# Optimization experiments

Measured on AMD Instinct MI355X. Metric: run time of the kernel, lower is better.

## Reference

```python
import jax, jax.numpy as jnp
import numpy as np

B, T, N = 4, 6, 1024          # patients, visits, diagnosis codes
CS, GS, H, AT, DA = 48, 32, 270, 32, 64  # code_size, graph_size, hidden, t_attention, dot-attn size
E, L, EV, ED = 32, 32, 20000, 400        # events/visit, event seq len, event vocab, event emb dim
OUT = 4000
INV_SQRT_AT = 1.0 / float(np.sqrt(AT))


def _w(k, shape, s=0.1):
    return jax.random.normal(k, shape, jnp.float32) * s


def setup_inputs():
    key = jax.random.key(0)
    ks = jax.random.split(key, 40)
    cat = jax.random.randint(ks[0], (B, T, N), 0, 4)  # disjoint m1/m2/m3 masks
    return {
        'code_x': jax.random.randint(ks[1], (B, T, N), 0, 2).astype(jnp.int32),
        'divided': jnp.stack([cat == 1, cat == 2, cat == 3], axis=-1).astype(jnp.int32),
        'neighbors': jax.random.randint(ks[2], (B, T, N), 0, 2).astype(jnp.int32),
        'lens': jnp.full((B,), T, dtype=jnp.int32),
        'events': jax.random.randint(ks[3], (B, T, E, L), 0, EV).astype(jnp.int32),
        'c_emb': _w(ks[4], (N, CS)),
        'n_emb': _w(ks[5], (N, CS)),
        'u_emb': _w(ks[6], (N, GS)),
        'adj': (jax.random.uniform(ks[7], (N, N)) < 0.02).astype(jnp.float32),
        'Wg': _w(ks[8], (CS, GS), 0.05), 'bg': jnp.zeros((GS,), jnp.float32),
        'gru_Wih': _w(ks[9], (GS, 3 * H), 0.05),
        'gru_Whh': _w(ks[10], (H, 3 * H), 0.05),
        'gru_bih': jnp.zeros((3 * H,), jnp.float32),
        'gru_bhh': jnp.zeros((3 * H,), jnp.float32),
        'Wq': _w(ks[11], (GS, AT), 0.05), 'bq': jnp.zeros((AT,), jnp.float32),
        'Wk': _w(ks[12], (GS, AT), 0.05), 'bk': jnp.zeros((AT,), jnp.float32),
        'Wv': _w(ks[13], (GS, H), 0.05), 'bv': jnp.zeros((H,), jnp.float32),
        'Wd': _w(ks[14], (H, DA), 0.05), 'bd': jnp.zeros((DA,), jnp.float32),
        'ctx': _w(ks[15], (DA,), 0.1),
        'Eemb': _w(ks[16], (EV, ED), 0.1),
        'lstm_Wih': _w(ks[17], (ED, 4 * H), 0.05),
        'lstm_Whh': _w(ks[18], (H, 4 * H), 0.05),
        'lstm_b': jnp.zeros((4 * H,), jnp.float32),
        'Wc': _w(ks[19], (H, OUT), 0.05),
        'bc': jnp.zeros((OUT,), jnp.float32),
    }


def _forward(code_x, divided, neighbors, events,
             c_emb, n_emb, u_emb, adj, Wg, bg,
             gru_Wih, gru_Whh, gru_bih, gru_bhh,
             Wq, bq, Wk, bk, Wv, bv,
             Wd, bd, ctx,
             Eemb, lstm_Wih, lstm_Whh, lstm_b,
             Wc, bc):
    Bsz, Tn, Nn = code_x.shape
    Hh = gru_Whh.shape[0]
    cx = code_x.astype(jnp.float32)
    nb = neighbors.astype(jnp.float32)
    dv = divided.astype(jnp.float32)

    def gru_cell(x, h):  # torch GRUCell: gates in (r, z, n) order
        gi = x @ gru_Wih + gru_bih
        gh = h @ gru_Whh + gru_bhh
        ir, iz, i_n = jnp.split(gi, 3, axis=-1)
        hr, hz, h_n = jnp.split(gh, 3, axis=-1)
        r = jax.nn.sigmoid(ir + hr)
        z = jax.nn.sigmoid(iz + hz)
        n = jnp.tanh(i_n + r * h_n)
        return (1.0 - z) * n + z * h

    def visit_step(carry, xs):
        h_prev, no_prev = carry
        t, c_t, n_t, d_t = xs  # c_t/n_t: [B,N], d_t: [B,N,3]
        cm = c_t[..., None]
        nm = n_t[..., None]
        # GraphLayer
        ce = cm * c_emb  # [B,N,CS]
        ne = nm * n_emb
        Ace = jnp.einsum('mn,bnc->bmc', adj, ce)
        Ane = jnp.einsum('mn,bnc->bmc', adj, ne)
        co = jax.nn.leaky_relu((ce + cm * Ace + cm * Ane) @ Wg + bg)  # [B,N,GS]
        no = jax.nn.leaky_relu((ne + nm * Ane + nm * Ace) @ Wg + bg)
        m1 = d_t[..., 0] > 0
        m2 = d_t[..., 1] > 0
        m3 = d_t[..., 2] > 0
        # TransitionLayer: persistent codes (m1) -> GRU, masked max-pool
        h_m1 = gru_cell(co, h_prev)  # [B,N,H]
        has1 = jnp.any(m1, axis=1, keepdims=True)
        mx1 = jnp.max(jnp.where(m1[..., None], h_m1, -jnp.inf), axis=1)
        out_m1 = jnp.where(has1, mx1, 0.0)
        # emerging (m2) / unrelated (m3) codes -> single-head attention over the m23 set
        m23 = m2 | m3
        q_in = jnp.where(m3[..., None], u_emb, no_prev)  # [B,N,GS]
        q = q_in @ Wq + bq
        k = co @ Wk + bk
        v = co @ Wv + bv
        g = jnp.einsum('bia,bja->bij', q, k) * INV_SQRT_AT  # [B,N,N]
        has23 = jnp.any(m23, axis=1)  # [B]
        g = jnp.where(m23[:, None, :], g, -jnp.inf)
        g = jnp.where(has23[:, None, None], g, 0.0)  # keep softmax finite when m23 empty
        score = jax.nn.softmax(g, axis=-1)
        h_m23 = jnp.tanh(jnp.einsum('bij,bjh->bih', score, v))  # [B,N,H]
        valid23 = (t > 0) & has23
        mx23 = jnp.max(jnp.where(m23[..., None], h_m23, -jnp.inf), axis=1)
        out_m23 = jnp.where(valid23[:, None], mx23, 0.0)
        h_new = jnp.where(m1[..., None], h_m1, 0.0)
        h_new = jnp.where(((t > 0) & m23)[..., None], h_m23, h_new)
        return (h_new, no), out_m1 + out_m23

    h0 = jnp.zeros((Bsz, Nn, Hh), jnp.float32)
    no0 = jnp.zeros((Bsz, Nn, GS), jnp.float32)
    xs = (jnp.arange(Tn), jnp.swapaxes(cx, 0, 1), jnp.swapaxes(nb, 0, 1), jnp.swapaxes(dv, 0, 1))
    _, outs = jax.lax.scan(visit_step, (h0, no0), xs)
    out_last = outs[-1]  # only the last visit's output survives the original loop

    # SentimentModel: embedding + LSTM over last visit's events (seqs == padded length L)
    x_emb = Eemb[events[:, -1]]  # [B,E,L,ED]

    def lstm_step(carry, x_t):  # torch LSTM gate order (i, f, g, o)
        h, c = carry
        gates = x_t @ lstm_Wih + h @ lstm_Whh + lstm_b
        i, f, gg, o = jnp.split(gates, 4, axis=-1)
        c = jax.nn.sigmoid(f) * c + jax.nn.sigmoid(i) * jnp.tanh(gg)
        h = jax.nn.sigmoid(o) * jnp.tanh(c)
        return (h, c), None

    hc0 = (jnp.zeros((Bsz, E, Hh), jnp.float32), jnp.zeros((Bsz, E, Hh), jnp.float32))
    (h_ev, _), _ = jax.lax.scan(lstm_step, hc0, jnp.moveaxis(x_emb, 2, 0))  # [B,E,H]

    def dp_attention(x):  # x: [B,M,H] -> [B,H]
        vu = (x @ Wd + bd) @ ctx  # [B,M]
        s = jax.nn.softmax(vu, axis=-1)
        return jnp.sum(x * s[..., None], axis=-2)

    stacked = jnp.concatenate([out_last[:, None, :], h_ev], axis=1)  # [B,1+E,H]
    o1 = dp_attention(stacked)
    o2 = dp_attention(o1[:, None, :])  # softmax over a singleton -> identity (as in source)
    return jax.nn.sigmoid(o2 @ Wc + bc)  # [B,OUT]


def reference(code_x, divided, neighbors, lens, events,
              c_emb, n_emb, u_emb, adj, Wg, bg,
              gru_Wih, gru_Whh, gru_bih, gru_bhh,
              Wq, bq, Wk, bk, Wv, bv,
              Wd, bd, ctx,
              Eemb, lstm_Wih, lstm_Whh, lstm_b,
              Wc, bc):
    # lens is all-T (fixed number of visits per patient in this reference)
    return _forward(code_x, divided, neighbors, events,
                    c_emb, n_emb, u_emb, adj, Wg, bg,
                    gru_Wih, gru_Whh, gru_bih, gru_bhh,
                    Wq, bq, Wk, bk, Wv, bv,
                    Wd, bd, ctx,
                    Eemb, lstm_Wih, lstm_Whh, lstm_b,
                    Wc, bc)
```

## Files before the change

kernel.cpp:

```cpp
#include <hip/hip_runtime.h>
#include <hip/hip_bf16.h>
#include <math.h>

#define Bc   4
#define Tc   6
#define Nc   1024
#define CSc  48
#define GSc  32
#define Hc   270
#define ATc  32
#define DAc  64
#define Ec   32
#define Lc   32
#define EDc  400
#define OUTc 4000
#define H3c  810
#define H4c  1080
#define BEc  128
#define KPE  416
#define KPG  64
#define KAB  320
#define NCMB 1382
#define NZCAP 96
#define INV_SQRT_AT_F 0.17677669529663687f
// ... 104 lines not shown
        for (int mi=0;mi<4;mi++) af[mi]  = *(const s8v*)&As[(wm+mi*16+lr)*40 + lk];
        #pragma unroll
        for (int ni=0;ni<4;ni++) bfr[ni] = *(const s8v*)&Bs[(wn+ni*16+lr)*40 + lk];
        #pragma unroll
        for (int mi=0;mi<4;mi++)
          #pragma unroll
          for (int ni=0;ni<4;ni++)
            acc[mi][ni] = __builtin_amdgcn_mfma_f32_16x16x32_bf16(af[mi], bfr[ni], acc[mi][ni], 0,0,0);
        __syncthreads();
    }

    #pragma unroll
    for (int mi=0;mi<4;mi++){
      #pragma unroll
      for (int ni=0;ni<4;ni++){
        int col = n0+wn+ni*16+lr;
        if (col >= N) continue;
        float bv_ = bias ? bias[col] : 0.0f;
        #pragma unroll
        for (int r=0;r<4;r++){
          int row = m0+wm+mi*16+lq*4+r;
          if (row >= M) continue;
          float x = acc[mi][ni][r] + bv_;
          if (EPIL == 0){
              float* C = (float*)P0;
              size_t base = (SPLITK>0) ? (size_t)z*(size_t)sC : 0;
              size_t grow = (SPLITK>0) ? (size_t)row : (size_t)z*M + row;
              C[base + grow*ldc + col] = x;
          } else if (EPIL == 1){
              x = (x>0.0f) ? x : 0.01f*x;
              if (row < 4096) ((ushort_t*)P0)[(size_t)row*KAB + col] = f2bf(x);
              else            ((ushort_t*)P1)[(size_t)(row-4096)*32 + col] = f2bf(x);
          } else if (EPIL == 5){
              if (col < 32)        ((ushort_t*)P0)[(size_t)row*32 + col] = f2bf(x);
              else if (col < 302)  ((ushort_t*)P1)[(size_t)(col-32)*4096 + row] = f2bf(x);
              else                 ((float*)P2)[(size_t)row*H4c + (col-302)] = x;
          }
        }
      }
    }
}

__global__ __launch_bounds__(256)
void attn_fused_kernel(const ushort_t* __restrict__ no_prev, const ushort_t* __restrict__ u_embb,
                       const float* __restrict__ Wq, const float* __restrict__ bq,
                       const ushort_t* __restrict__ kb, const ushort_t* __restrict__ vT,
                       const int* __restrict__ divided, const float* __restrict__ hm1,
                       ushort_t* __restrict__ Abuf, float* __restrict__ hm23,
                       int t, int wr23)
{
    __shared__ float    scs[16*1028];
    __shared__ ushort_t stg[288*72];
    __shared__ ushort_t Qs[16*40];
    __shared__ float    qinS[16*33];
    __shared__ float    WqS[32*33];
    __shared__ float    mskS[1024];
    __shared__ float    rowmax[16], rowinv[16], hasS[4];

    const int rt = blockIdx.x;
    const int b  = blockIdx.y;
    const int tid = threadIdx.x;
    const int w = tid>>6, l = tid&63, lr = l&15, lq = l>>4;
    const int lk8 = lq*8;
    const int row0 = rt*16;
    const size_t gq = (size_t)b*Nc + row0;

    bool lany = false;
    #pragma unroll
    for (int c4=0;c4<4;c4++){
        int c = tid*4 + c4;
        const int* dv = divided + (((size_t)b*Tc + t)*Nc + c)*3;
        bool m23 = (dv[1]>0)||(dv[2]>0);
        mskS[c] = m23 ? 1.0f : 0.0f;
        lany |= m23;
    }
    if (l==0) hasS[w] = 0.0f;
    bool wany = __any(lany);
    if (l==0) hasS[w] = wany ? 1.0f : 0.0f;

    for (int i=tid;i<16*32;i+=256){
        int r = i>>5, j = i&31;
        int n = row0 + r;
        bool m3 = divided[(((size_t)b*Tc+t)*Nc+n)*3+2] > 0;
        qinS[r*33+j] = m3 ? b2f(u_embb[(size_t)n*GSc+j]) : b2f(no_prev[(gq+r)*GSc+j]);
    }
    for (int i=tid;i<32*32;i+=256){
        int j=i>>5, o=i&31;
        WqS[j*33+o] = Wq[(size_t)j*ATc+o];
    }
    __syncthreads();
    const bool has = (hasS[0]+hasS[1]+hasS[2]+hasS[3]) > 0.5f;

    {
        int r = tid>>4, o2 = (tid&15)*2;
        float a0 = bq[o2], a1 = bq[o2+1];
        for (int j=0;j<32;j++){
            float q = qinS[r*33+j];
            a0 += q*WqS[j*33+o2];
            a1 += q*WqS[j*33+o2+1];
        }
        Qs[r*40+o2]   = f2bf(a0);
        Qs[r*40+o2+1] = f2bf(a1);
    }
    __syncthreads();

    for (int kt=0;kt<8;kt++){
        #pragma unroll
        for (int i2=0;i2<2;i2++){
            int idx = tid*2+i2;
            int kr = idx>>2, seg = idx&3;
            *(uint4*)&stg[kr*40 + seg*8] =
                *(const uint4*)(kb + ((size_t)b*Nc + kt*128 + kr)*GSc + seg*8);
        }
        __syncthreads();
        s8v af = *(const s8v*)&Qs[lr*40 + lk8];
        #pragma unroll
        for (int ni=0;ni<2;ni++){
            int nt = w*2 + ni;
            s8v bf = *(const s8v*)&stg[(nt*16+lr)*40 + lk8];
            f4v a0 = (f4v){0,0,0,0};
            a0 = __builtin_amdgcn_mfma_f32_16x16x32_bf16(af, bf, a0, 0,0,0);
            #pragma unroll
            for (int r2=0;r2<4;r2++)
                scs[(lq*4+r2)*1028 + kt*128 + nt*16 + lr] = a0[r2];
        }
        __syncthreads();
    }

    {
        int r = tid>>4, i = tid&15;
        if (has){
            float m = -INFINITY;
            for (int j=0;j<64;j++){
                int c = i + 16*j;
                if (mskS[c] > 0.5f) m = fmaxf(m, scs[r*1028+c]*INV_SQRT_AT_F);
            }
            #pragma unroll
            for (int o=1;o<16;o<<=1) m = fmaxf(m, __shfl_xor(m, o, 64));
            if (i==0) rowmax[r] = m;
        }
        __syncthreads();
        float gm = has ? rowmax[r] : 0.0f;
        float s = 0.0f;
        for (int j=0;j<64;j++){
            int c = i + 16*j;
            float p;
            if (has) p = (mskS[c]>0.5f) ? expf(scs[r*1028+c]*INV_SQRT_AT_F - gm) : 0.0f;
            else     p = 1.0f;
            scs[r*1028+c] = p;
            s += p;
        }
        #pragma unroll
        for (int o=1;o<16;o<<=1) s += __shfl_xor(s, o, 64);
        if (i==0) rowinv[r] = 1.0f/s;
    }
    for (int i=tid;i<18*72;i+=256)
        stg[(270+(i/72))*72 + (i%72)] = 0;
    __syncthreads();
    const float inv = rowinv[lr];

    f4v acc[5];
    #pragma unroll
    for (int j=0;j<5;j++) acc[j] = (f4v){0,0,0,0};
    for (int vc=0;vc<16;vc++){
        for (int idx=tid; idx<2160; idx+=256){
            int n = idx>>3, seg = idx&7;
            *(uint4*)&stg[n*72 + seg*8] =
                *(const uint4*)(vT + (size_t)n*(Bc*Nc) + (size_t)b*Nc + vc*64 + seg*8);
        }
        __syncthreads();
        #pragma unroll
        for (int ki=0;ki<2;ki++){
            int kbase = vc*64 + ki*32 + lk8;
            u16x8 a16;
            #pragma unroll
            for (int e=0;e<8;e++) a16[e] = f2bf(scs[lr*1028 + kbase + e] * inv);
            s8v af = *(s8v*)&a16;
            #pragma unroll
            for (int j=0;j<5;j++){
                int nt = w + 4*j;
                if (nt < 18){
                    s8v bf = *(const s8v*)&stg[(nt*16+lr)*72 + ki*32 + lk8];
                    acc[j] = __builtin_amdgcn_mfma_f32_16x16x32_bf16(af, bf, acc[j], 0,0,0);
                }
            }
        }
        __syncthreads();
    }

    #pragma unroll
    for (int j=0;j<5;j++){
        int nt = w + 4*j;
        if (nt >= 18) continue;
        int col = nt*16 + lr;
        if (col >= Hc) continue;
        #pragma unroll
        for (int r2=0;r2<4;r2++){
            int row16 = lq*4 + r2;
            size_t grow = gq + row16;
            int n = row0 + row16;
            const int* dv = divided + (((size_t)b*Tc + t)*Nc + n)*3;
            bool m1  = dv[0]>0;
            bool m23 = (dv[1]>0)||(dv[2]>0);
            float xt = tanhf(acc[j][r2]);
            float hv = m23 ? xt : (m1 ? hm1[grow*Hc + col] : 0.0f);
            Abuf[grow*KAB + 32 + col] = f2bf(hv);
            if (wr23) hm23[grow*Hc + col] = xt;
        }
    }
}

template<int ACT>
__global__ __launch_bounds__(256)
void gemm_kernel(const float* __restrict__ A, const float* __restrict__ Bm,
                 const float* __restrict__ bias, float* __restrict__ C,
                 int M, int Nn, int K)
{
    constexpr int BM=64, BN=64, BK=16;
    __shared__ float As[BK][BM+4];
    __shared__ float Bs[BK][BN+4];
    const int row0 = blockIdx.y*BM, col0 = blockIdx.x*BN;
    const int tid = threadIdx.x;
    const int tr = (tid>>4)<<2;
    const int tc = (tid&15)<<2;
    const int ar = tid>>2;
    const int ac = (tid&3)<<2;
    const int br = tid>>4;
    const int bc = (tid&15)<<2;
    float acc[4][4] = {};
    for (int k0=0;k0<K;k0+=BK){
        #pragma unroll
        for (int i=0;i<4;i++){
            int gr=row0+ar, gc=k0+ac+i;
            As[ac+i][ar] = (gr<M && gc<K) ? A[(size_t)gr*K+gc] : 0.0f;
        }
        #pragma unroll
        for (int i=0;i<4;i++){
// ... 3 lines not shown
        __syncthreads();
        #pragma unroll
        for (int kk=0;kk<BK;kk++){
            float a0=As[kk][tr+0], a1=As[kk][tr+1], a2=As[kk][tr+2], a3=As[kk][tr+3];
            float b0=Bs[kk][tc+0], b1=Bs[kk][tc+1], b2=Bs[kk][tc+2], b3=Bs[kk][tc+3];
            acc[0][0]+=a0*b0; acc[0][1]+=a0*b1; acc[0][2]+=a0*b2; acc[0][3]+=a0*b3;
            acc[1][0]+=a1*b0; acc[1][1]+=a1*b1; acc[1][2]+=a1*b2; acc[1][3]+=a1*b3;
            acc[2][0]+=a2*b0; acc[2][1]+=a2*b1; acc[2][2]+=a2*b2; acc[2][3]+=a2*b3;
            acc[3][0]+=a3*b0; acc[3][1]+=a3*b1; acc[3][2]+=a3*b2; acc[3][3]+=a3*b3;
        }
        __syncthreads();
    }
    #pragma unroll
    for (int i=0;i<4;i++){
        int r=row0+tr+i; if (r>=M) continue;
        #pragma unroll
        for (int j=0;j<4;j++){
            int c=col0+tc+j; if (c>=Nn) continue;
            float x = acc[i][j];
            if (bias) x += bias[c];
            if (ACT==3) x = 1.0f/(1.0f+expf(-x));
            C[(size_t)r*Nn+c] = x;
        }
    }
}

#define PR0 32768LL
#define PR1 2048LL
#define PR3 442240LL
#define PR4 1382LL
#define PR5 449280LL
#define PR6 313344LL
#define PR7 73728LL
#define PR8 36864LL
#define PR9 1310720LL
#define PRTOT (PR0+PR1+PR3+PR4+PR5+PR6+PR7+PR8+PR9)

__global__ void prep_kernel(const float* __restrict__ u_emb,
                            const float* __restrict__ Wg,
                            const float* __restrict__ Wk, const float* __restrict__ Wv,
                            const float* __restrict__ gru_Wih, const float* __restrict__ gru_Whh,
                            const float* __restrict__ bk, const float* __restrict__ bv,
                            const float* __restrict__ gru_bih, const float* __restrict__ gru_bhh,
                            const float* __restrict__ lstm_Wih, const float* __restrict__ lstm_Whh,
                            ushort_t* u_embb, ushort_t* WgT,
                            ushort_t* WB, float* biasB, ushort_t* WTl, ushort_t* WhhRT,
                            ushort_t* hbLA, ushort_t* hbLB, float* cst, ushort_t* Abuf)
{
    long long idx = (long long)blockIdx.x*256 + threadIdx.x;
    if (idx < PR0){ u_embb[idx] = f2bf(u_emb[idx]); return; } idx -= PR0;
    if (idx < PR1){ int n=(int)(idx>>6), k=(int)(idx&63);
        WgT[idx] = (k<CSc) ? f2bf(Wg[(size_t)k*GSc+n]) : (ushort_t)0; return; } idx -= PR1;
    if (idx < PR3){
        int n=(int)(idx/KAB), k=(int)(idx%KAB);
        float v = 0.0f;
        if (n < 32){            if (k<32) v = Wk[(size_t)k*ATc + n]; }
        else if (n < 302){      if (k<32) v = Wv[(size_t)k*Hc + (n-32)]; }
        else if (n < 572){ int j=n-302;
            if (k<32) v = gru_Wih[(size_t)k*H3c + j];
            else if (k<302) v = gru_Whh[(size_t)(k-32)*H3c + j]; }
        else if (n < 842){ int j=(n-572)+270;
            if (k<32) v = gru_Wih[(size_t)k*H3c + j];
            else if (k<302) v = gru_Whh[(size_t)(k-32)*H3c + j]; }
        else if (n < 1112){ int j=(n-842)+540;
            if (k<32) v = gru_Wih[(size_t)k*H3c + j]; }
        else { int j=(n-1112)+540;
            if (k>=32 && k<302) v = gru_Whh[(size_t)(k-32)*H3c + j]; }
        WB[idx] = f2bf(v); return; } idx -= PR3;
    if (idx < PR4){
        int n = (int)idx; float v;
        if (n < 32)        v = bk[n];
        else if (n < 302)  v = bv[n-32];
        else if (n < 572)  v = gru_bih[n-302] + gru_bhh[n-302];
        else if (n < 842)  v = gru_bih[(n-572)+270] + gru_bhh[(n-572)+270];
        else if (n < 1112) v = gru_bih[(n-842)+540];
        else               v = gru_bhh[(n-1112)+540];
        biasB[n] = v; return; } idx -= PR4;
    if (idx < PR5){ int n=(int)(idx/KPE), k=(int)(idx%KPE);
        WTl[idx] = (k<EDc) ? f2bf(lstm_Wih[(size_t)k*H4c+n]) : (ushort_t)0; return; } idx -= PR5;
    if (idx < PR6){
        int jg=(int)(idx/(64*288)); int r2=(int)(idx%(64*288));
        int n=r2/288, k=r2%288;
        int gate=n>>4, jj=n&15, j=jg*16+jj;
        WhhRT[idx] = (k<Hc && j<Hc) ? f2bf(lstm_Whh[(size_t)k*H4c + gate*Hc + j]) : (ushort_t)0;
        return; } idx -= PR6;
    if (idx < PR7){ if (idx < 36864) hbLA[idx] = 0; else hbLB[idx-36864] = 0; return; } idx -= PR7;
    if (idx < PR8){ cst[idx] = 0.0f; return; } idx -= PR8;
    if (idx < PR9){ Abuf[idx] = 0; }
}

__global__ void nz_build_kernel(const float* __restrict__ adj, int* __restrict__ nzc,
                                int* __restrict__ nzidx)
{
    int n = blockIdx.x;
    __shared__ int cnt;
    if (threadIdx.x == 0) cnt = 0;
    __syncthreads();
    for (int k = threadIdx.x; k < Nc; k += 256){
        if (adj[(size_t)n*Nc + k] != 0.0f){
            int pos = atomicAdd(&cnt, 1);
            if (pos < NZCAP) nzidx[(size_t)n*NZCAP + pos] = k;
        }
    }
    __syncthreads();
    if (threadIdx.x == 0) nzc[n] = (cnt < NZCAP) ? cnt : NZCAP;
}

__global__ __launch_bounds__(192)
void s_sparse_kernel(const int* __restrict__ code_x, const int* __restrict__ neighbors,
                     const float* __restrict__ c_emb, const float* __restrict__ n_emb,
                     const int* __restrict__ nzc, const int* __restrict__ nzidx,
                     int t, float* __restrict__ S)
{
    int n = blockIdx.x;
    int tid = threadIdx.x;
    int b = tid / CSc, c = tid % CSc;
    int cnt = nzc[n];
    float s = 0.0f;
    for (int i=0; i<cnt; i++){
        int k = nzidx[(size_t)n*NZCAP + i];
        int cm = code_x  [((size_t)b*Tc+t)*Nc + k];
// ... 43 lines not shown
{
    int nc = blockIdx.x, b = blockIdx.y;
    int j = threadIdx.x;
    if (j >= Hc) return;
    float m1v = -INFINITY, m23v = -INFINITY;
    #pragma unroll 4
    for (int n = nc*32; n < nc*32+32; n++){
        const int* dv = divided + (((size_t)b*Tc + (Tc-1))*Nc + n)*3;
        bool m1  = dv[0] > 0;
        bool m23 = (dv[1] > 0) || (dv[2] > 0);
        size_t o = ((size_t)b*Nc+n)*Hc + j;
        if (m1)  m1v  = fmaxf(m1v,  hm1[o]);
        if (m23) m23v = fmaxf(m23v, hm23[o]);
    }
    part1 [((size_t)b*32+nc)*320 + j] = m1v;
    part23[((size_t)b*32+nc)*320 + j] = m23v;
}

__global__ __launch_bounds__(320)
void outlast_combine_kernel(const float* __restrict__ part1, const float* __restrict__ part23,
                            float* __restrict__ outlast)
{
    int b = blockIdx.x; int j = threadIdx.x;
    if (j >= Hc) return;
    float a = -INFINITY, c = -INFINITY;
    for (int nc=0;nc<32;nc++){
        a = fmaxf(a, part1 [((size_t)b*32+nc)*320 + j]);
        c = fmaxf(c, part23[((size_t)b*32+nc)*320 + j]);
    }
    outlast[(size_t)b*Hc + j] = (a==-INFINITY ? 0.0f : a) + (c==-INFINITY ? 0.0f : c);
}

__global__ __launch_bounds__(256)
void lstm_step_mfma(const float* __restrict__ gx,
                    const ushort_t* __restrict__ WhhRT,
                    const ushort_t* __restrict__ hb_in,
                    ushort_t* __restrict__ hb_out,
                    float* __restrict__ cst,
                    float* __restrict__ hev_out)
{
    int cg = blockIdx.x & 3, jg = blockIdx.x >> 2;
    int tid = threadIdx.x;
    int w = tid>>6, l = tid&63;
    int mi = w>>1, ni0 = (w&1)*2;
    int arow = cg*32 + mi*16 + (l&15);
    int koff = (l>>4)*8;
    const ushort_t* Wb = WhhRT + (size_t)jg*64*288;

    f4v acc0 = (f4v){0,0,0,0}, acc1 = (f4v){0,0,0,0};
    #pragma unroll
    for (int k0=0;k0<288;k0+=32){
        s8v a  = *(const s8v*)(hb_in + (size_t)arow*288 + k0 + koff);
        s8v b0 = *(const s8v*)(Wb + (size_t)(ni0*16 + (l&15))*288 + k0 + koff);
        s8v b1 = *(const s8v*)(Wb + (size_t)((ni0+1)*16 + (l&15))*288 + k0 + koff);
        acc0 = __builtin_amdgcn_mfma_f32_16x16x32_bf16(a, b0, acc0, 0,0,0);
        acc1 = __builtin_amdgcn_mfma_f32_16x16x32_bf16(a, b1, acc1, 0,0,0);
    }
    __shared__ float gs[32][64];
    int crow = mi*16 + (l>>4)*4;
    int ccol = l&15;
    #pragma unroll
    for (int r=0;r<4;r++){
        gs[crow+r][ni0*16 + ccol]     = acc0[r];
        gs[crow+r][(ni0+1)*16 + ccol] = acc1[r];
    }
    __syncthreads();
    #pragma unroll
    for (int p=0;p<2;p++){
        int idx = tid + p*256;
        int cl = idx>>4, jj = idx&15;
        int j = jg*16 + jj;
        if (j < Hc){
            int cell = cg*32 + cl;
            const float* g = gx + (size_t)cell*H4c;
            float ig = sigmoid_f(gs[cl][jj]      + g[j]);
            float fg = sigmoid_f(gs[cl][16+jj]   + g[Hc+j]);
            float gg = tanhf    (gs[cl][32+jj]   + g[2*Hc+j]);
            float og = sigmoid_f(gs[cl][48+jj]   + g[3*Hc+j]);
            size_t co = (size_t)cell*288 + j;
            float cn = fg*cst[co] + ig*gg;
            cst[co] = cn;
            float hn = og*tanhf(cn);
            hb_out[co] = f2bf(hn);
            if (hev_out) hev_out[(size_t)cell*Hc + j] = hn;
        }
    }
}

__global__ __launch_bounds__(256)
void heads_kernel(const float* __restrict__ outlast, const float* __restrict__ hev,
                  const float* __restrict__ Wd, const float* __restrict__ bd,
                  const float* __restrict__ ctx, float* __restrict__ o1)
{
    int b = blockIdx.x, tid = threadIdx.x;
    __shared__ float wdc[Hc+1];
    __shared__ float sc[Ec+1];
    for (int j=tid;j<Hc;j+=256){
        float s = 0.0f;
        for (int d=0;d<DAc;d++) s += Wd[(size_t)j*DAc+d]*ctx[d];
        wdc[j] = s;
    }
    if (tid == 255){
        float s = 0.0f;
        for (int d=0;d<DAc;d++) s += bd[d]*ctx[d];
        wdc[Hc] = s;
    }
    __syncthreads();
    if (tid < Ec+1){
        const float* x = (tid==0) ? (outlast + (size_t)b*Hc)
                                  : (hev + ((size_t)b*Ec + tid-1)*Hc);
        float s = wdc[Hc];
        for (int j=0;j<Hc;j++) s += x[j]*wdc[j];
        sc[tid] = s;
    }
    __syncthreads();
    if (tid == 0){
        float m = -INFINITY;
// ... 28 lines not shown
    const float* gru_Wih   = (const float*)d_in[11];
    const float* gru_Whh   = (const float*)d_in[12];
    const float* gru_bih   = (const float*)d_in[13];
    const float* gru_bhh   = (const float*)d_in[14];
    const float* Wq        = (const float*)d_in[15];
    const float* bq        = (const float*)d_in[16];
    const float* Wk        = (const float*)d_in[17];
    const float* bk        = (const float*)d_in[18];
    const float* Wv        = (const float*)d_in[19];
    const float* bv        = (const float*)d_in[20];
    const float* Wd        = (const float*)d_in[21];
    const float* bd        = (const float*)d_in[22];
    const float* ctx       = (const float*)d_in[23];
    const float* Eemb      = (const float*)d_in[24];
    const float* lstm_Wih  = (const float*)d_in[25];
    const float* lstm_Whh  = (const float*)d_in[26];
    const float* lstm_b    = (const float*)d_in[27];
    const float* Wc        = (const float*)d_in[28];
    const float* bc        = (const float*)d_in[29];
    float* out = (float*)d_out;

    float* ws = (float*)d_ws;
    size_t off = 0;
    auto alloc = [&](size_t n){ n = (n+7)&~(size_t)7; float* p = ws + off; off += n; return p; };
    auto allocU = [&](size_t n){ return (ushort_t*)alloc((n+1)/2); };

    float* hm1     = alloc((size_t)Bc*Nc*Hc);
    float* hm23    = alloc((size_t)Bc*Nc*Hc);
    float* S       = alloc((size_t)Nc*Bc*CSc);
    float* gsum    = alloc((size_t)Bc*Nc*H4c);
    ushort_t* Abuf  = allocU((size_t)Bc*Nc*KAB);
    ushort_t* noA   = allocU((size_t)Bc*Nc*GSc);
    ushort_t* noB   = allocU((size_t)Bc*Nc*GSc);
    ushort_t* kb    = allocU((size_t)Bc*Nc*ATc);
    ushort_t* vT    = allocU((size_t)Hc*Bc*Nc);
    ushort_t* u_embb= allocU((size_t)Nc*GSc);
    ushort_t* WgT   = allocU((size_t)GSc*KPG);
    ushort_t* WB    = allocU((size_t)NCMB*KAB);
    ushort_t* WTl   = allocU((size_t)H4c*KPE);
    ushort_t* WhhRT = allocU((size_t)17*64*288);
    ushort_t* hbLA  = allocU((size_t)BEc*288);
    ushort_t* hbLB  = allocU((size_t)BEc*288);
    float* cst     = alloc((size_t)BEc*288);
    float* biasB   = alloc((size_t)NCMB);
    int*   nzc     = (int*)alloc((size_t)Nc);
    int*   nzidx   = (int*)alloc((size_t)Nc*NZCAP);
    float* outlast = alloc((size_t)Bc*Hc);
    float* o1      = alloc((size_t)Bc*Hc);
    float* hev     = alloc((size_t)BEc*Hc);
    float* part1   = alloc((size_t)Bc*32*320);
    float* part23  = alloc((size_t)Bc*32*320);

    float* gatesx  = gsum;
    (void)ws_size; (void)in_sizes; (void)n_in; (void)out_size;

    {
        long long nb = (PRTOT + 255) / 256;
        prep_kernel<<<dim3((unsigned)nb), dim3(256), 0, stream>>>(
            u_emb, Wg, Wk, Wv, gru_Wih, gru_Whh, bk, bv, gru_bih, gru_bhh,
            lstm_Wih, lstm_Whh,
            u_embb, WgT, WB, biasB, WTl, WhhRT, hbLA, hbLB, cst, Abuf);
        nz_build_kernel<<<dim3(Nc), dim3(256), 0, stream>>>(adj, nzc, nzidx);
    }

    ushort_t* no_prev = noB;
    ushort_t* no_cur  = noA;
    for (int t=0; t<Tc; t++){
        s_sparse_kernel<<<dim3(Nc), dim3(192), 0, stream>>>(code_x, neighbors, c_emb, n_emb,
                                                            nzc, nzidx, t, S);
        mfma_k<1,0,2><<<dim3(1,64,1),256,0,stream>>>(
            (const ushort_t*)c_emb, WgT, bg,
            Abuf, no_cur, (void*)n_emb, S, code_x, neighbors,
            2*Bc*Nc, GSc, KPG, 0, KPG, 0, 0,0,0, t);
        mfma_k<5,0,0><<<dim3(11,32,1),256,0,stream>>>(
            Abuf, WB, biasB,
            kb, vT, gsum, nullptr, nullptr, nullptr,
            Bc*Nc, NCMB, KAB, KAB, KAB, 0, 0,0,0, 0);
        if (t == 0){
            gru_combine_t0_kernel<<<dim3(Bc*Nc), dim3(256), 0, stream>>>(gsum, divided, Abuf);
        } else {
            gru_combine_kernel<<<dim3(Bc*Nc), dim3(256), 0, stream>>>(gsum, Abuf, hm1);
            attn_fused_kernel<<<dim3(64, Bc), dim3(256), 0, stream>>>(
                no_prev, u_embb, Wq, bq, kb, vT, divided, hm1,
                Abuf, hm23, t, (t == Tc-1) ? 1 : 0);
            if (t == Tc-1){
                outlast_partial_kernel<<<dim3(32, Bc), dim3(320), 0, stream>>>(divided, hm1, hm23, part1, part23);
                outlast_combine_kernel<<<dim3(Bc), dim3(320), 0, stream>>>(part1, part23, outlast);
            }
        }
        ushort_t* tmp = no_prev; no_prev = no_cur; no_cur = tmp;
    }

    mfma_k<0,0,3><<<dim3(9,32,1),256,0,stream>>>(
        nullptr, WTl, lstm_b,
        gatesx, nullptr, nullptr, Eemb, events, nullptr,
        BEc*Lc, H4c, KPE, 0, KPE, H4c, 0,0,0, 0);
    {
        ushort_t* hin = hbLA; ushort_t* hout = hbLB;
        for (int l=0; l<Lc; l++){
            lstm_step_mfma<<<dim3(68), dim3(256), 0, stream>>>(
                gatesx + (size_t)l*BEc*H4c, WhhRT, hin, hout, cst,
                (l == Lc-1) ? hev : nullptr);
            ushort_t* tmp = hin; hin = hout; hout = tmp;
        }
    }

    heads_kernel<<<dim3(Bc), dim3(256), 0, stream>>>(outlast, hev, Wd, bd, ctx, o1);
    {
        dim3 grid((OUTc+63)/64, 1, 1);
        gemm_kernel<3><<<grid,dim3(256),0,stream>>>(o1, Wc, bc, out, Bc, OUTc, Hc);
    }
}
```

Measured before the change: 1.201 ms.

## Fuse LSTM steps into a persistent kernel with grid barrier; precompute bf16 softmax probs

Replaces the 32 per-step LSTM kernel launches with one persistent 68-block kernel. It keeps the recurrent weights and cell state in registers and synchronises steps through a global atomic-counter barrier, removing launch overhead and the cell-state round trip to global memory. The attention kernel now folds the 1/sqrt scale into the score store. It keeps the row max and sum in registers instead of shared memory plus a barrier, and pre-packs the normalised probabilities to bf16 in shared memory once rather than converting inside the PV loop. The spin barrier assumes all 68 blocks are co-resident, and the counter is reset only by the prep kernel on each call.

```diff
diff --git a/kernel.cpp b/kernel.cpp
--- a/kernel.cpp
+++ b/kernel.cpp
@@ -179,11 +179,12 @@
 {
     __shared__ float    scs[16*1028];
     __shared__ ushort_t stg[288*72];
+    __shared__ ushort_t Pb[32*16*40];
     __shared__ ushort_t Qs[16*40];
-    __shared__ float    qinS[16*33];
-    __shared__ float    WqS[32*33];
     __shared__ float    mskS[1024];
-    __shared__ float    rowmax[16], rowinv[16], hasS[4];
+    __shared__ float    hasS[4];
+    float* qinS = (float*)Pb;
+    float* WqS  = (float*)&Pb[1056];
 
     const int rt = blockIdx.x;
     const int b  = blockIdx.y;
@@ -202,9 +203,10 @@
         mskS[c] = m23 ? 1.0f : 0.0f;
         lany |= m23;
     }
-    if (l==0) hasS[w] = 0.0f;
     bool wany = __any(lany);
     if (l==0) hasS[w] = wany ? 1.0f : 0.0f;
+
+    for (int i=tid; i<18*72; i+=256) stg[270*72 + i] = 0;
 
     for (int i=tid;i<16*32;i+=256){
         int r = i>>5, j = i&31;
@@ -250,46 +252,49 @@
             a0 = __builtin_amdgcn_mfma_f32_16x16x32_bf16(af, bf, a0, 0,0,0);
             #pragma unroll
             for (int r2=0;r2<4;r2++)
-                scs[(lq*4+r2)*1028 + kt*128 + nt*16 + lr] = a0[r2];
+                scs[(lq*4+r2)*1028 + kt*128 + nt*16 + lr] = a0[r2]*INV_SQRT_AT_F;
         }
         __syncthreads();
     }
 
     {
         int r = tid>>4, i = tid&15;
+        float m = -INFINITY;
         if (has){
-            float m = -INFINITY;
             for (int j=0;j<64;j++){
                 int c = i + 16*j;
-                if (mskS[c] > 0.5f) m = fmaxf(m, scs[r*1028+c]*INV_SQRT_AT_F);
+                if (mskS[c] > 0.5f) m = fmaxf(m, scs[r*1028+c]);
             }
             #pragma unroll
             for (int o=1;o<16;o<<=1) m = fmaxf(m, __shfl_xor(m, o, 64));
-            if (i==0) rowmax[r] = m;
-        }
-        __syncthreads();
-        float gm = has ? rowmax[r] : 0.0f;
+        }
+        float gm = has ? m : 0.0f;
         float s = 0.0f;
         for (int j=0;j<64;j++){
             int c = i + 16*j;
             float p;
-            if (has) p = (mskS[c]>0.5f) ? expf(scs[r*1028+c]*INV_SQRT_AT_F - gm) : 0.0f;
+            if (has) p = (mskS[c]>0.5f) ? expf(scs[r*1028+c]-gm) : 0.0f;
             else     p = 1.0f;
             scs[r*1028+c] = p;
             s += p;
         }
         #pragma unroll
         for (int o=1;o<16;o<<=1) s += __shfl_xor(s, o, 64);
-        if (i==0) rowinv[r] = 1.0f/s;
-    }
-    for (int i=tid;i<18*72;i+=256)
-        stg[(270+(i/72))*72 + (i%72)] = 0;
+        float inv = 1.0f/s;
+        #pragma unroll 4
+        for (int j2=0;j2<32;j2++){
+            int c = 2*i + 32*j2;
+            float p0 = scs[r*1028+c]*inv;
+            float p1 = scs[r*1028+c+1]*inv;
+            unsigned int pk = (unsigned int)f2bf(p0) | ((unsigned int)f2bf(p1)<<16);
+            *(unsigned int*)&Pb[(size_t)j2*640 + r*40 + 2*i] = pk;
+        }
+    }
     __syncthreads();
-    const float inv = rowinv[lr];
 
     f4v acc[5];
     #pragma unroll
-    for (int j=0;j<5;j++) acc[j] = (f4v){0,0,0,0};
+    for (int j5=0;j5<5;j5++) acc[j5] = (f4v){0,0,0,0};
     for (int vc=0;vc<16;vc++){
         for (int idx=tid; idx<2160; idx+=256){
             int n = idx>>3, seg = idx&7;
@@ -299,17 +304,14 @@
         __syncthreads();
         #pragma unroll
         for (int ki=0;ki<2;ki++){
-            int kbase = vc*64 + ki*32 + lk8;
-            u16x8 a16;
+            int chunk = vc*2 + ki;
+            s8v af = *(const s8v*)&Pb[(size_t)chunk*640 + lr*40 + lk8];
             #pragma unroll
-            for (int e=0;e<8;e++) a16[e] = f2bf(scs[lr*1028 + kbase + e] * inv);
-            s8v af = *(s8v*)&a16;
-            #pragma unroll
-            for (int j=0;j<5;j++){
-                int nt = w + 4*j;
+            for (int j5=0;j5<5;j5++){
+                int nt = w + 4*j5;
                 if (nt < 18){
                     s8v bf = *(const s8v*)&stg[(nt*16+lr)*72 + ki*32 + lk8];
-                    acc[j] = __builtin_amdgcn_mfma_f32_16x16x32_bf16(af, bf, acc[j], 0,0,0);
+                    acc[j5] = __builtin_amdgcn_mfma_f32_16x16x32_bf16(af, bf, acc[j5], 0,0,0);
                 }
             }
         }
@@ -317,8 +319,8 @@
     }
 
     #pragma unroll
-    for (int j=0;j<5;j++){
-        int nt = w + 4*j;
+    for (int j5=0;j5<5;j5++){
+        int nt = w + 4*j5;
         if (nt >= 18) continue;
         int col = nt*16 + lr;
         if (col >= Hc) continue;
@@ -330,7 +332,7 @@
             const int* dv = divided + (((size_t)b*Tc + t)*Nc + n)*3;
             bool m1  = dv[0]>0;
             bool m23 = (dv[1]>0)||(dv[2]>0);
-            float xt = tanhf(acc[j][r2]);
+            float xt = tanhf(acc[j5][r2]);
             float hv = m23 ? xt : (m1 ? hm1[grow*Hc + col] : 0.0f);
             Abuf[grow*KAB + 32 + col] = f2bf(hv);
             if (wr23) hm23[grow*Hc + col] = xt;
@@ -400,7 +402,7 @@
 #define PR5 449280LL
 #define PR6 313344LL
 #define PR7 73728LL
-#define PR8 36864LL
+#define PR8 8LL
 #define PR9 1310720LL
 #define PRTOT (PR0+PR1+PR3+PR4+PR5+PR6+PR7+PR8+PR9)
 
@@ -413,7 +415,7 @@
                             const float* __restrict__ lstm_Wih, const float* __restrict__ lstm_Whh,
                             ushort_t* u_embb, ushort_t* WgT,
                             ushort_t* WB, float* biasB, ushort_t* WTl, ushort_t* WhhRT,
-                            ushort_t* hbLA, ushort_t* hbLB, float* cst, ushort_t* Abuf)
+                            ushort_t* hbLA, ushort_t* hbLB, unsigned int* bar, ushort_t* Abuf)
 {
     long long idx = (long long)blockIdx.x*256 + threadIdx.x;
     if (idx < PR0){ u_embb[idx] = f2bf(u_emb[idx]); return; } idx -= PR0;
@@ -453,7 +455,7 @@
         WhhRT[idx] = (k<Hc && j<Hc) ? f2bf(lstm_Whh[(size_t)k*H4c + gate*Hc + j]) : (ushort_t)0;
         return; } idx -= PR6;
     if (idx < PR7){ if (idx < 36864) hbLA[idx] = 0; else hbLB[idx-36864] = 0; return; } idx -= PR7;
-    if (idx < PR8){ cst[idx] = 0.0f; return; } idx -= PR8;
+    if (idx < PR8){ bar[idx] = 0u; return; } idx -= PR8;
     if (idx < PR9){ Abuf[idx] = 0; }
 }
 
@@ -564,12 +566,11 @@
 }
 
 __global__ __launch_bounds__(256)
-void lstm_step_mfma(const float* __restrict__ gx,
-                    const ushort_t* __restrict__ WhhRT,
-                    const ushort_t* __restrict__ hb_in,
-                    ushort_t* __restrict__ hb_out,
-                    float* __restrict__ cst,
-                    float* __restrict__ hev_out)
+void lstm_persist(const float* __restrict__ gx_all,
+                  const ushort_t* __restrict__ WhhRT,
+                  ushort_t* __restrict__ hbA, ushort_t* __restrict__ hbB,
+                  unsigned int* __restrict__ bar,
+                  float* __restrict__ hev_out)
 {
     int cg = blockIdx.x & 3, jg = blockIdx.x >> 2;
     int tid = threadIdx.x;
@@ -579,42 +580,73 @@
     int koff = (l>>4)*8;
     const ushort_t* Wb = WhhRT + (size_t)jg*64*288;
 
-    f4v acc0 = (f4v){0,0,0,0}, acc1 = (f4v){0,0,0,0};
+    s8v bf0[9], bf1[9];
     #pragma unroll
-    for (int k0=0;k0<288;k0+=32){
-        s8v a  = *(const s8v*)(hb_in + (size_t)arow*288 + k0 + koff);
-        s8v b0 = *(const s8v*)(Wb + (size_t)(ni0*16 + (l&15))*288 + k0 + koff);
-        s8v b1 = *(const s8v*)(Wb + (size_t)((ni0+1)*16 + (l&15))*288 + k0 + koff);
-        acc0 = __builtin_amdgcn_mfma_f32_16x16x32_bf16(a, b0, acc0, 0,0,0);
-        acc1 = __builtin_amdgcn_mfma_f32_16x16x32_bf16(a, b1, acc1, 0,0,0);
-    }
+    for (int kc=0;kc<9;kc++){
+        bf0[kc] = *(const s8v*)(Wb + (size_t)(ni0*16 + (l&15))*288 + kc*32 + koff);
+        bf1[kc] = *(const s8v*)(Wb + (size_t)((ni0+1)*16 + (l&15))*288 + kc*32 + koff);
+    }
+
     __shared__ float gs[32][64];
-    int crow = mi*16 + (l>>4)*4;
-    int ccol = l&15;
-    #pragma unroll
-    for (int r=0;r<4;r++){
-        gs[crow+r][ni0*16 + ccol]     = acc0[r];
-        gs[crow+r][(ni0+1)*16 + ccol] = acc1[r];
-    }
-    __syncthreads();
-    #pragma unroll
-    for (int p=0;p<2;p++){
-        int idx = tid + p*256;
-        int cl = idx>>4, jj = idx&15;
-        int j = jg*16 + jj;
-        if (j < Hc){
-            int cell = cg*32 + cl;
-            const float* g = gx + (size_t)cell*H4c;
-            float ig = sigmoid_f(gs[cl][jj]      + g[j]);
-            float fg = sigmoid_f(gs[cl][16+jj]   + g[Hc+j]);
-            float gg = tanhf    (gs[cl][32+jj]   + g[2*Hc+j]);
-            float og = sigmoid_f(gs[cl][48+jj]   + g[3*Hc+j]);
-            size_t co = (size_t)cell*288 + j;
-            float cn = fg*cst[co] + ig*gg;
-            cst[co] = cn;
-            float hn = og*tanhf(cn);
-            hb_out[co] = f2bf(hn);
-            if (hev_out) hev_out[(size_t)cell*Hc + j] = hn;
+    int cl0 = tid>>4, jj0 = tid&15;
+    int j = jg*16 + jj0;
+    bool jok = (j < Hc);
+    float c0 = 0.0f, c1 = 0.0f;
+    int crow = mi*16 + (l>>4)*4, ccol = l&15;
+
+    for (int st=0; st<Lc; st++){
+        const ushort_t* hin  = (st&1) ? hbB : hbA;
+        ushort_t*       hout = (st&1) ? hbA : hbB;
+        const float* gx = gx_all + (size_t)st*BEc*H4c;
+
+        f4v acc0=(f4v){0,0,0,0}, acc1=(f4v){0,0,0,0};
+        #pragma unroll
+        for (int kc=0;kc<9;kc++){
+            s8v a = *(const s8v*)(hin + (size_t)arow*288 + kc*32 + koff);
+            acc0 = __builtin_amdgcn_mfma_f32_16x16x32_bf16(a, bf0[kc], acc0, 0,0,0);
+            acc1 = __builtin_amdgcn_mfma_f32_16x16x32_bf16(a, bf1[kc], acc1, 0,0,0);
+        }
+        #pragma unroll
+        for (int r=0;r<4;r++){
+            gs[crow+r][ni0*16 + ccol]     = acc0[r];
+            gs[crow+r][(ni0+1)*16 + ccol] = acc1[r];
+        }
+        __syncthreads();
+        if (jok){
+            {
+                int cell = cg*32 + cl0;
+                const float* g = gx + (size_t)cell*H4c;
+                float ig = sigmoid_f(gs[cl0][jj0]    + g[j]);
+                float fg = sigmoid_f(gs[cl0][16+jj0] + g[Hc+j]);
+                float gg = tanhf    (gs[cl0][32+jj0] + g[2*Hc+j]);
+                float og = sigmoid_f(gs[cl0][48+jj0] + g[3*Hc+j]);
+                float cn = fg*c0 + ig*gg; c0 = cn;
+                float hn = og*tanhf(cn);
+                hout[(size_t)cell*288 + j] = f2bf(hn);
+                if (st == Lc-1) hev_out[(size_t)cell*Hc + j] = hn;
+            }
+            {
+                int cell = cg*32 + 16 + cl0;
+                const float* g = gx + (size_t)cell*H4c;
+                float ig = sigmoid_f(gs[16+cl0][jj0]    + g[j]);
+                float fg = sigmoid_f(gs[16+cl0][16+jj0] + g[Hc+j]);
+                float gg = tanhf    (gs[16+cl0][32+jj0] + g[2*Hc+j]);
+                float og = sigmoid_f(gs[16+cl0][48+jj0] + g[3*Hc+j]);
+                float cn = fg*c1 + ig*gg; c1 = cn;
+                float hn = og*tanhf(cn);
+                hout[(size_t)cell*288 + j] = f2bf(hn);
+                if (st == Lc-1) hev_out[(size_t)cell*Hc + j] = hn;
+            }
+        }
+        __syncthreads();
+        if (st < Lc-1){
+            if (tid == 0){
+                __hip_atomic_fetch_add(bar, 1u, __ATOMIC_ACQ_REL, __HIP_MEMORY_SCOPE_AGENT);
+                unsigned int tgt = 68u*(unsigned)(st+1);
+                while (__hip_atomic_load(bar, __ATOMIC_ACQUIRE, __HIP_MEMORY_SCOPE_AGENT) < tgt)
+                    __builtin_amdgcn_s_sleep(2);
+            }
+            __syncthreads();
         }
     }
 }
@@ -718,7 +750,7 @@
     ushort_t* WhhRT = allocU((size_t)17*64*288);
     ushort_t* hbLA  = allocU((size_t)BEc*288);
     ushort_t* hbLB  = allocU((size_t)BEc*288);
-    float* cst     = alloc((size_t)BEc*288);
+    unsigned int* bar = (unsigned int*)alloc(8);
     float* biasB   = alloc((size_t)NCMB);
     int*   nzc     = (int*)alloc((size_t)Nc);
     int*   nzidx   = (int*)alloc((size_t)Nc*NZCAP);
@@ -736,7 +768,7 @@
         prep_kernel<<<dim3((unsigned)nb), dim3(256), 0, stream>>>(
             u_emb, Wg, Wk, Wv, gru_Wih, gru_Whh, bk, bv, gru_bih, gru_bhh,
             lstm_Wih, lstm_Whh,
-            u_embb, WgT, WB, biasB, WTl, WhhRT, hbLA, hbLB, cst, Abuf);
+            u_embb, WgT, WB, biasB, WTl, WhhRT, hbLA, hbLB, bar, Abuf);
         nz_build_kernel<<<dim3(Nc), dim3(256), 0, stream>>>(adj, nzc, nzidx);
     }
 
@@ -772,15 +804,7 @@
         nullptr, WTl, lstm_b,
         gatesx, nullptr, nullptr, Eemb, events, nullptr,
         BEc*Lc, H4c, KPE, 0, KPE, H4c, 0,0,0, 0);
-    {
-        ushort_t* hin = hbLA; ushort_t* hout = hbLB;
-        for (int l=0; l<Lc; l++){
-            lstm_step_mfma<<<dim3(68), dim3(256), 0, stream>>>(
-                gatesx + (size_t)l*BEc*H4c, WhhRT, hin, hout, cst,
-                (l == Lc-1) ? hev : nullptr);
-            ushort_t* tmp = hin; hin = hout; hout = tmp;
-        }
-    }
+    lstm_persist<<<dim3(68), dim3(256), 0, stream>>>(gatesx, WhhRT, hbLA, hbLB, bar, hev);
 
     heads_kernel<<<dim3(Bc), dim3(256), 0, stream>>>(outlast, hev, Wd, bd, ctx, o1);
     {
```

Measured after the change: 1.294 ms. 7.8% more time.

## Pre-swizzle K/V into MFMA fragment layout and keep attention scores in registers

Applied to the files above, without the earlier changes.

The projection GEMM epilogue now writes K and V directly in the per-lane MFMA fragment order, so the attention kernel loads operands straight from global memory without LDS staging and its barriers. Scores stay in registers for the softmax, with cross-wave max and sum reductions done through a small shared array, and probabilities are written once as bf16 to LDS for the PV product. This cuts LDS use and synchronisation but scatters the epilogue stores, and it needs an extra zero-init of the padded V buffer in the prep kernel.

```diff
diff --git a/kernel.cpp b/kernel.cpp
--- a/kernel.cpp
+++ b/kernel.cpp
@@ -160,9 +160,17 @@
               if (row < 4096) ((ushort_t*)P0)[(size_t)row*KAB + col] = f2bf(x);
               else            ((ushort_t*)P1)[(size_t)(row-4096)*32 + col] = f2bf(x);
           } else if (EPIL == 5){
-              if (col < 32)        ((ushort_t*)P0)[(size_t)row*32 + col] = f2bf(x);
-              else if (col < 302)  ((ushort_t*)P1)[(size_t)(col-32)*4096 + row] = f2bf(x);
-              else                 ((float*)P2)[(size_t)row*H4c + (col-302)] = x;
+              int b2 = row>>10, rh = row&1023;
+              if (col < 32){
+                  int kt = rh>>7, nt_=(rh>>4)&7, lrK=rh&15, lqK=col>>3, e=col&7;
+                  ((ushort_t*)P0)[((((size_t)b2*8+kt)*8+nt_)*64 + lqK*16+lrK)*8 + e] = f2bf(x);
+              } else if (col < 302){
+                  int vd = col-32;
+                  int c = rh>>5, lqV=(rh>>3)&3, e=rh&7, nt=vd>>4, lrV=vd&15;
+                  ((ushort_t*)P1)[((((size_t)b2*32+c)*18+nt)*64 + lqV*16+lrV)*8 + e] = f2bf(x);
+              } else {
+                  ((float*)P2)[(size_t)row*H4c + (col-302)] = x;
+              }
           }
         }
       }
@@ -172,18 +180,18 @@
 __global__ __launch_bounds__(256)
 void attn_fused_kernel(const ushort_t* __restrict__ no_prev, const ushort_t* __restrict__ u_embb,
                        const float* __restrict__ Wq, const float* __restrict__ bq,
-                       const ushort_t* __restrict__ kb, const ushort_t* __restrict__ vT,
+                       const ushort_t* __restrict__ kSw, const ushort_t* __restrict__ vSw,
                        const int* __restrict__ divided, const float* __restrict__ hm1,
                        ushort_t* __restrict__ Abuf, float* __restrict__ hm23,
                        int t, int wr23)
 {
-    __shared__ float    scs[16*1028];
-    __shared__ ushort_t stg[288*72];
+    __shared__ ushort_t Pb[32*16*40];
     __shared__ ushort_t Qs[16*40];
-    __shared__ float    qinS[16*33];
-    __shared__ float    WqS[32*33];
     __shared__ float    mskS[1024];
-    __shared__ float    rowmax[16], rowinv[16], hasS[4];
+    __shared__ float    redS[4][16];
+    __shared__ float    hasS[4];
+    float* qinS = (float*)Pb;
+    float* WqS  = (float*)&Pb[1056];
 
     const int rt = blockIdx.x;
     const int b  = blockIdx.y;
@@ -202,7 +210,6 @@
         mskS[c] = m23 ? 1.0f : 0.0f;
         lany |= m23;
     }
-    if (l==0) hasS[w] = 0.0f;
     bool wany = __any(lany);
     if (l==0) hasS[w] = wany ? 1.0f : 0.0f;
 
@@ -232,93 +239,109 @@
     }
     __syncthreads();
 
-    for (int kt=0;kt<8;kt++){
-        #pragma unroll
-        for (int i2=0;i2<2;i2++){
-            int idx = tid*2+i2;
-            int kr = idx>>2, seg = idx&3;
-            *(uint4*)&stg[kr*40 + seg*8] =
-                *(const uint4*)(kb + ((size_t)b*Nc + kt*128 + kr)*GSc + seg*8);
-        }
-        __syncthreads();
-        s8v af = *(const s8v*)&Qs[lr*40 + lk8];
-        #pragma unroll
-        for (int ni=0;ni<2;ni++){
-            int nt = w*2 + ni;
-            s8v bf = *(const s8v*)&stg[(nt*16+lr)*40 + lk8];
-            f4v a0 = (f4v){0,0,0,0};
-            a0 = __builtin_amdgcn_mfma_f32_16x16x32_bf16(af, bf, a0, 0,0,0);
-            #pragma unroll
-            for (int r2=0;r2<4;r2++)
-                scs[(lq*4+r2)*1028 + kt*128 + nt*16 + lr] = a0[r2];
-        }
-        __syncthreads();
-    }
-
-    {
-        int r = tid>>4, i = tid&15;
-        if (has){
-            float m = -INFINITY;
-            for (int j=0;j<64;j++){
-                int c = i + 16*j;
-                if (mskS[c] > 0.5f) m = fmaxf(m, scs[r*1028+c]*INV_SQRT_AT_F);
+    s8v af = *(const s8v*)&Qs[lr*40 + lk8];
+    s8v kf[8][2];
+    #pragma unroll
+    for (int kt=0;kt<8;kt++)
+      #pragma unroll
+      for (int ni=0;ni<2;ni++)
+        kf[kt][ni] = *(const s8v*)(kSw + ((((size_t)b*8+kt)*8 + (w*2+ni))*64 + l)*8);
+    f4v qk[8][2];
+    #pragma unroll
+    for (int kt=0;kt<8;kt++)
+      #pragma unroll
+      for (int ni=0;ni<2;ni++){
+        f4v zz = (f4v){0,0,0,0};
+        qk[kt][ni] = __builtin_amdgcn_mfma_f32_16x16x32_bf16(af, kf[kt][ni], zz, 0,0,0);
+      }
+
+    float rmax[4] = {-INFINITY,-INFINITY,-INFINITY,-INFINITY};
+    #pragma unroll
+    for (int kt=0;kt<8;kt++)
+      #pragma unroll
+      for (int ni=0;ni<2;ni++){
+        int colb = kt*128 + (w*2+ni)*16 + lr;
+        float mk = mskS[colb];
+        #pragma unroll
+        for (int r2=0;r2<4;r2++){
+            float v = qk[kt][ni][r2]*INV_SQRT_AT_F;
+            qk[kt][ni][r2] = v;
+            if (mk > 0.5f) rmax[r2] = fmaxf(rmax[r2], v);
+        }
+      }
+    #pragma unroll
+    for (int o=1;o<16;o<<=1)
+      #pragma unroll
+      for (int r2=0;r2<4;r2++) rmax[r2] = fmaxf(rmax[r2], __shfl_xor(rmax[r2], o, 64));
+    if (lr==0){
+        #pragma unroll
+        for (int r2=0;r2<4;r2++) redS[w][lq*4+r2] = rmax[r2];
+    }
+    __syncthreads();
+    float gm[4], inv[4];
+    #pragma unroll
+    for (int r2=0;r2<4;r2++){
+        float m = fmaxf(fmaxf(redS[0][lq*4+r2], redS[1][lq*4+r2]),
+                        fmaxf(redS[2][lq*4+r2], redS[3][lq*4+r2]));
+        gm[r2] = m;
+    }
+    float rs[4] = {0,0,0,0};
+    #pragma unroll
+    for (int kt=0;kt<8;kt++)
+      #pragma unroll
+      for (int ni=0;ni<2;ni++){
+        int colb = kt*128 + (w*2+ni)*16 + lr;
+        float mk = mskS[colb];
+        #pragma unroll
+        for (int r2=0;r2<4;r2++){
+            float p = (mk > 0.5f) ? expf(qk[kt][ni][r2] - gm[r2]) : 0.0f;
+            qk[kt][ni][r2] = p;
+            rs[r2] += p;
+        }
+      }
+    #pragma unroll
+    for (int o=1;o<16;o<<=1)
+      #pragma unroll
+      for (int r2=0;r2<4;r2++) rs[r2] += __shfl_xor(rs[r2], o, 64);
+    __syncthreads();
+    if (lr==0){
+        #pragma unroll
+        for (int r2=0;r2<4;r2++) redS[w][lq*4+r2] = rs[r2];
+    }
+    __syncthreads();
+    #pragma unroll
+    for (int r2=0;r2<4;r2++){
+        float s = redS[0][lq*4+r2] + redS[1][lq*4+r2] + redS[2][lq*4+r2] + redS[3][lq*4+r2];
+        inv[r2] = has ? 1.0f/s : 0.0f;
+    }
+
+    #pragma unroll
+    for (int kt=0;kt<8;kt++)
+      #pragma unroll
+      for (int ni=0;ni<2;ni++)
+        #pragma unroll
+        for (int r2=0;r2<4;r2++)
+            Pb[(kt*4+w)*640 + (lq*4+r2)*40 + ni*16+lr] = f2bf(qk[kt][ni][r2]*inv[r2]);
+    __syncthreads();
+
+    f4v acc[5];
+    #pragma unroll
+    for (int j5=0;j5<5;j5++) acc[j5] = (f4v){0,0,0,0};
+    for (int c=0;c<32;c++){
+        s8v pa = *(const s8v*)&Pb[c*640 + lr*40 + lk8];
+        #pragma unroll
+        for (int j5=0;j5<5;j5++){
+            int nt = w + 4*j5;
+            if (nt < 18){
+                s8v vf = *(const s8v*)(vSw + ((((size_t)b*32+c)*18 + nt)*64 + l)*8);
+                acc[j5] = __builtin_amdgcn_mfma_f32_16x16x32_bf16(pa, vf, acc[j5], 0,0,0);
             }
-            #pragma unroll
-            for (int o=1;o<16;o<<=1) m = fmaxf(m, __shfl_xor(m, o, 64));
-            if (i==0) rowmax[r] = m;
-        }
-        __syncthreads();
-        float gm = has ? rowmax[r] : 0.0f;
-        float s = 0.0f;
-        for (int j=0;j<64;j++){
-            int c = i + 16*j;
-            float p;
-            if (has) p = (mskS[c]>0.5f) ? expf(scs[r*1028+c]*INV_SQRT_AT_F - gm) : 0.0f;
-            else     p = 1.0f;
-            scs[r*1028+c] = p;
-            s += p;
-        }
-        #pragma unroll
-        for (int o=1;o<16;o<<=1) s += __shfl_xor(s, o, 64);
-        if (i==0) rowinv[r] = 1.0f/s;
-    }
-    for (int i=tid;i<18*72;i+=256)
-        stg[(270+(i/72))*72 + (i%72)] = 0;
-    __syncthreads();
-    const float inv = rowinv[lr];
-
-    f4v acc[5];
-    #pragma unroll
-    for (int j=0;j<5;j++) acc[j] = (f4v){0,0,0,0};
-    for (int vc=0;vc<16;vc++){
-        for (int idx=tid; idx<2160; idx+=256){
-            int n = idx>>3, seg = idx&7;
-            *(uint4*)&stg[n*72 + seg*8] =
-                *(const uint4*)(vT + (size_t)n*(Bc*Nc) + (size_t)b*Nc + vc*64 + seg*8);
-        }
-        __syncthreads();
-        #pragma unroll
-        for (int ki=0;ki<2;ki++){
-            int kbase = vc*64 + ki*32 + lk8;
-            u16x8 a16;
-            #pragma unroll
-            for (int e=0;e<8;e++) a16[e] = f2bf(scs[lr*1028 + kbase + e] * inv);
-            s8v af = *(s8v*)&a16;
-            #pragma unroll
-            for (int j=0;j<5;j++){
-                int nt = w + 4*j;
-                if (nt < 18){
-                    s8v bf = *(const s8v*)&stg[(nt*16+lr)*72 + ki*32 + lk8];
-                    acc[j] = __builtin_amdgcn_mfma_f32_16x16x32_bf16(af, bf, acc[j], 0,0,0);
-                }
-            }
-        }
-        __syncthreads();
-    }
-
-    #pragma unroll
-    for (int j=0;j<5;j++){
-        int nt = w + 4*j;
+        }
+    }
+
+    #pragma unroll
+    for (int j5=0;j5<5;j5++){
+        int nt = w + 4*j5;
         if (nt >= 18) continue;
         int col = nt*16 + lr;
         if (col >= Hc) continue;
@@ -330,7 +353,7 @@
             const int* dv = divided + (((size_t)b*Tc + t)*Nc + n)*3;
             bool m1  = dv[0]>0;
             bool m23 = (dv[1]>0)||(dv[2]>0);
-            float xt = tanhf(acc[j][r2]);
+            float xt = tanhf(acc[j5][r2]);
             float hv = m23 ? xt : (m1 ? hm1[grow*Hc + col] : 0.0f);
             Abuf[grow*KAB + 32 + col] = f2bf(hv);
             if (wr23) hm23[grow*Hc + col] = xt;
@@ -402,7 +425,8 @@
 #define PR7 73728LL
 #define PR8 36864LL
 #define PR9 1310720LL
-#define PRTOT (PR0+PR1+PR3+PR4+PR5+PR6+PR7+PR8+PR9)
+#define PR10 1179648LL
+#define PRTOT (PR0+PR1+PR3+PR4+PR5+PR6+PR7+PR8+PR9+PR10)
 
 __global__ void prep_kernel(const float* __restrict__ u_emb,
                             const float* __restrict__ Wg,
@@ -413,7 +437,8 @@
                             const float* __restrict__ lstm_Wih, const float* __restrict__ lstm_Whh,
                             ushort_t* u_embb, ushort_t* WgT,
                             ushort_t* WB, float* biasB, ushort_t* WTl, ushort_t* WhhRT,
-                            ushort_t* hbLA, ushort_t* hbLB, float* cst, ushort_t* Abuf)
+                            ushort_t* hbLA, ushort_t* hbLB, float* cst, ushort_t* Abuf,
+                            ushort_t* vSw)
 {
     long long idx = (long long)blockIdx.x*256 + threadIdx.x;
     if (idx < PR0){ u_embb[idx] = f2bf(u_emb[idx]); return; } idx -= PR0;
@@ -454,7 +479,8 @@
         return; } idx -= PR6;
     if (idx < PR7){ if (idx < 36864) hbLA[idx] = 0; else hbLB[idx-36864] = 0; return; } idx -= PR7;
     if (idx < PR8){ cst[idx] = 0.0f; return; } idx -= PR8;
-    if (idx < PR9){ Abuf[idx] = 0; }
+    if (idx < PR9){ Abuf[idx] = 0; return; } idx -= PR9;
+    if (idx < PR10){ vSw[idx] = 0; }
 }
 
 __global__ void nz_build_kernel(const float* __restrict__ adj, int* __restrict__ nzc,
@@ -709,8 +735,8 @@
     ushort_t* Abuf  = allocU((size_t)Bc*Nc*KAB);
     ushort_t* noA   = allocU((size_t)Bc*Nc*GSc);
     ushort_t* noB   = allocU((size_t)Bc*Nc*GSc);
-    ushort_t* kb    = allocU((size_t)Bc*Nc*ATc);
-    ushort_t* vT    = allocU((size_t)Hc*Bc*Nc);
+    ushort_t* kSw   = allocU((size_t)Bc*Nc*ATc);
+    ushort_t* vSw   = allocU((size_t)Bc*32*18*64*8);
     ushort_t* u_embb= allocU((size_t)Nc*GSc);
     ushort_t* WgT   = allocU((size_t)GSc*KPG);
     ushort_t* WB    = allocU((size_t)NCMB*KAB);
@@ -736,7 +762,7 @@
         prep_kernel<<<dim3((unsigned)nb), dim3(256), 0, stream>>>(
             u_emb, Wg, Wk, Wv, gru_Wih, gru_Whh, bk, bv, gru_bih, gru_bhh,
             lstm_Wih, lstm_Whh,
-            u_embb, WgT, WB, biasB, WTl, WhhRT, hbLA, hbLB, cst, Abuf);
+            u_embb, WgT, WB, biasB, WTl, WhhRT, hbLA, hbLB, cst, Abuf, vSw);
         nz_build_kernel<<<dim3(Nc), dim3(256), 0, stream>>>(adj, nzc, nzidx);
     }
 
@@ -751,14 +777,14 @@
             2*Bc*Nc, GSc, KPG, 0, KPG, 0, 0,0,0, t);
         mfma_k<5,0,0><<<dim3(11,32,1),256,0,stream>>>(
             Abuf, WB, biasB,
-            kb, vT, gsum, nullptr, nullptr, nullptr,
+            kSw, vSw, gsum, nullptr, nullptr, nullptr,
             Bc*Nc, NCMB, KAB, KAB, KAB, 0, 0,0,0, 0);
         if (t == 0){
             gru_combine_t0_kernel<<<dim3(Bc*Nc), dim3(256), 0, stream>>>(gsum, divided, Abuf);
         } else {
             gru_combine_kernel<<<dim3(Bc*Nc), dim3(256), 0, stream>>>(gsum, Abuf, hm1);
             attn_fused_kernel<<<dim3(64, Bc), dim3(256), 0, stream>>>(
-                no_prev, u_embb, Wq, bq, kb, vT, divided, hm1,
+                no_prev, u_embb, Wq, bq, kSw, vSw, divided, hm1,
                 Abuf, hm23, t, (t == Tc-1) ? 1 : 0);
             if (t == Tc-1){
                 outlast_partial_kernel<<<dim3(32, Bc), dim3(320), 0, stream>>>(divided, hm1, hm23, part1, part23);
```

Measured after the change: 1.055 ms. 12.2% less time.
